# Kernel tuning notes

Measured on AMD Instinct MI355X. Metric: run time of the kernel, lower is better.

## Reference

```python
import jax, jax.numpy as jnp
import numpy as np

SPARSE_SHAPE = (468, 468, 1)
WINDOW_SHAPE = (12, 12, 1)
POS_TEMPERATURE = 10000.0
DROP_RANGE = (16, 32, 64, 100000)
DROP_TOKENS = (16, 32, 64, 144)
BATCH_SIZE = 4

_NX = int(np.ceil(SPARSE_SHAPE[0] / WINDOW_SHAPE[0])) + 1
_NY = int(np.ceil(SPARSE_SHAPE[1] / WINDOW_SHAPE[1])) + 1
_NZ = int(np.ceil(SPARSE_SHAPE[2] / WINDOW_SHAPE[2])) + 1
NUM_WINDOWS = BATCH_SIZE * _NX * _NY * _NZ  # total window-index space


def get_window_coors(coords, do_shift):
    # coords: [N,4] int32, order (b, z, y, x)
    wx, wy, wz = WINDOW_SHAPE
    if do_shift:
        sx, sy, sz = wx // 2, wy // 2, wz // 2
    else:
        sx, sy, sz = wx, wy, wz
    if SPARSE_SHAPE[2] == wz:
        sz = 0
    cx = coords[:, 3] + sx
    cy = coords[:, 2] + sy
    cz = coords[:, 1] + sz
    win_x, win_y, win_z = cx // wx, cy // wy, cz // wz
    per_sample = _NX * _NY * _NZ
    batch_win_inds = coords[:, 0] * per_sample + win_x * (_NY * _NZ) + win_y * _NZ + win_z
    coors_in_win = jnp.stack([cz % wz, cy % wy, cx % wx], axis=-1)  # (z,y,x)
    return batch_win_inds, coors_in_win


def masked_inner_win_inds(win_inds, keep):
    # rank (0..cnt-1) of each KEPT voxel inside its window (stable order)
    n = win_inds.shape[0]
    sentinel = jnp.int32(NUM_WINDOWS + 1)
    key = jnp.where(keep, win_inds, sentinel)
    order = jnp.argsort(key, stable=True)
    sk = key[order]
    pos = jnp.arange(n, dtype=jnp.int32)
    new_seg = jnp.concatenate([jnp.ones((1,), bool), sk[1:] != sk[:-1]])
    seg_start = jax.lax.cummax(jnp.where(new_seg, pos, 0), axis=0)
    inner_sorted = pos - seg_start
    return jnp.zeros(n, jnp.int32).at[order].set(inner_sorted)


def drop_single_shift(win_inds, keep):
    counts = jax.ops.segment_sum(keep.astype(jnp.int32), win_inds, num_segments=NUM_WINDOWS)
    num_before = counts[win_inds]  # tokens per window before this drop
    inner = masked_inner_win_inds(win_inds, keep)
    target = jnp.zeros_like(win_inds)
    drop_lvl = -jnp.ones_like(win_inds)
    lower = 0
    for dl, (upper, max_tok) in enumerate(zip(DROP_RANGE, DROP_TOKENS)):
        m = (num_before >= lower) & (num_before < upper)
        target = jnp.where(m, max_tok, target)
        drop_lvl = jnp.where(m, dl, drop_lvl)
        lower = upper
    keep_new = keep & (inner < target)
    return keep_new, jnp.where(keep, drop_lvl, -1), jnp.where(keep, inner, -1)


def pos_embed(coords_in_win, feat_dim):
    # 2D branch: window_shape[-1] == 1
    wx, wy, _ = WINDOW_SHAPE
    y = coords_in_win[:, 1].astype(jnp.float32) - wy / 2
    x = coords_in_win[:, 2].astype(jnp.float32) - wx / 2
    pos_length = feat_dim // 2
    inv_freq = POS_TEMPERATURE ** ((jnp.arange(pos_length // 2, dtype=jnp.float32) * 2) / pos_length)
    ex = x[:, None] / inv_freq[None, :]
    ey = y[:, None] / inv_freq[None, :]
    ex = jnp.stack([jnp.sin(ex), jnp.cos(ex)], axis=-1).reshape(x.shape[0], -1)
    ey = jnp.stack([jnp.sin(ey), jnp.cos(ey)], axis=-1).reshape(y.shape[0], -1)
    return jnp.concatenate([ex, ey], axis=-1)  # [N, feat_dim], gap == 0


def setup_inputs() -> dict:
    key = jax.random.key(0)
    k1, k2, k3, k4 = jax.random.split(key, 4)
    N, C = 300000, 128
    b = jax.random.randint(k1, (N,), 0, BATCH_SIZE, dtype=jnp.int32)
    z = jnp.zeros((N,), jnp.int32)
    y = jax.random.randint(k2, (N,), 0, SPARSE_SHAPE[1], dtype=jnp.int32)
    x = jax.random.randint(k3, (N,), 0, SPARSE_SHAPE[0], dtype=jnp.int32)
    voxel_coords = jnp.stack([b, z, y, x], axis=-1)
    voxel_feat = jax.random.normal(k4, (N, C), dtype=jnp.float32)
    return {"voxel_feat": voxel_feat, "voxel_coords": voxel_coords}


def reference(voxel_feat, voxel_coords):
    coords = voxel_coords.astype(jnp.int32)
    win0, inwin0 = get_window_coors(coords, do_shift=False)
    win1, inwin1 = get_window_coors(coords, do_shift=True)
    keep = jnp.ones(coords.shape[0], bool)
    keep, dl0, inner0 = drop_single_shift(win0, keep)
    keep, dl1, inner1 = drop_single_shift(win1, keep)
    C = voxel_feat.shape[1]
    pe0 = pos_embed(inwin0, C).astype(voxel_feat.dtype)
    pe1 = pos_embed(inwin1, C).astype(voxel_feat.dtype)
    # static-shape stand-in for boolean filtering: mask instead of compact
    feat_kept = voxel_feat * keep[:, None].astype(voxel_feat.dtype)
    return (feat_kept, keep, win0, win1, dl0, dl1, inner0, inner1, pe0, pe1)
```

## Files before the change

kernel.cpp:

```cpp
#include <hip/hip_runtime.h>

#define NWIN 12800
#define PER_SAMPLE 3200
#define NY_NZ 80
#define NZW 2

using f4 = __attribute__((ext_vector_type(4))) float;

__device__ __forceinline__ void tgt_lvl(int nb, int& tgt, int& lvl) {
    if (nb < 16)          { tgt = 16;  lvl = 0; }
    else if (nb < 32)     { tgt = 32;  lvl = 1; }
    else if (nb < 64)     { tgt = 64;  lvl = 2; }
    else                  { tgt = 144; lvl = 3; }
}

__global__ void k_pe_wins(const int4* __restrict__ coords, int N,
                          int* __restrict__ w0, int* __restrict__ w1,
                          int* __restrict__ counts0, f4* __restrict__ out4) {
    int tid = blockIdx.x * blockDim.x + threadIdx.x;
    if (tid >= N * 16) return;
    int i    = tid >> 4;
    int c4   = tid & 15;
    int lane = threadIdx.x & 63;

    int x = 0, y = 0;
    if (c4 == 0) {
        int4 c = coords[i];
        x = c.w; y = c.z;
        int wi0 = c.x * PER_SAMPLE + ((x + 12) / 12) * NY_NZ + ((y + 12) / 12) * NZW + c.y;
        int wi1 = c.x * PER_SAMPLE + ((x + 6)  / 12) * NY_NZ + ((y + 6)  / 12) * NZW + c.y;
        w0[i] = wi0;
        w1[i] = wi1;
        atomicAdd(&counts0[wi0], 1);
    }
    int src = lane & 48;
    x = __shfl(x, src, 64);
    y = __shfl(y, src, 64);

    float x0 = (float)(x % 12) - 6.0f;
    float y0 = (float)(y % 12) - 6.0f;
    float x1 = (float)((x + 6) % 12) - 6.0f;
    float y1 = (float)((y + 6) % 12) - 6.0f;

    float rf0 = exp2f((float)(2 * c4) * -0.415241011860920285f);
    float rf1 = rf0 * 0.749894209332455847f;

    float ax0 = x0 * rf0, bx0 = x0 * rf1, ay0 = y0 * rf0, by0 = y0 * rf1;
    float ax1 = x1 * rf0, bx1 = x1 * rf1, ay1 = y1 * rf0, by1 = y1 * rf1;
    f4 p0x = { __sinf(ax0), __cosf(ax0), __sinf(bx0), __cosf(bx0) };
    f4 p0y = { __sinf(ay0), __cosf(ay0), __sinf(by0), __cosf(by0) };
    f4 p1x = { __sinf(ax1), __cosf(ax1), __sinf(bx1), __cosf(bx1) };
    f4 p1y = { __sinf(ay1), __cosf(ay1), __sinf(by1), __cosf(by1) };

    size_t pe0 = ((size_t)N * 135) >> 2;
    size_t pe1 = pe0 + (((size_t)N * 128) >> 2);
    size_t vb  = (size_t)i * 32 + c4;
    __builtin_nontemporal_store(p0x, &out4[pe0 + vb]);
    __builtin_nontemporal_store(p0y, &out4[pe0 + vb + 16]);
    __builtin_nontemporal_store(p1x, &out4[pe1 + vb]);
    __builtin_nontemporal_store(p1y, &out4[pe1 + vb + 16]);
}

__global__ void k_scan(const int* __restrict__ counts,
                       int* __restrict__ starts, int* __restrict__ cursor) {
    __shared__ int ssum[256];
    const int CH = NWIN / 256;
    int t = threadIdx.x;
    int base = t * CH;
    int s = 0;
    for (int k = 0; k < CH; ++k) s += counts[base + k];
    ssum[t] = s;
    __syncthreads();
    for (int off = 1; off < 256; off <<= 1) {
        int v = (t >= off) ? ssum[t - off] : 0;
        __syncthreads();
        ssum[t] += v;
        __syncthreads();
    }
    int run = ssum[t] - s;
    for (int k = 0; k < CH; ++k) {
        starts[base + k] = run;
        cursor[base + k] = run;
        run += counts[base + k];
    }
}

__global__ void k_scatter0(const int* __restrict__ w0, int N,
                           int* __restrict__ cursor, int* __restrict__ sorted) {
    int i = blockIdx.x * blockDim.x + threadIdx.x;
    if (i >= N) return;
    int pos = atomicAdd(&cursor[w0[i]], 1);
    sorted[pos] = i;
}

__global__ void k_rank(const int* __restrict__ starts, const int* __restrict__ counts,
                       const int* __restrict__ sorted, int* __restrict__ inner,
                       const int* __restrict__ w1, int* __restrict__ counts1) {
    __shared__ int seg[1024];
    int w = blockIdx.x;
    int L = counts[w];
    if (L == 0) return;
    int s = starts[w];
    int lane = threadIdx.x;
    int tgt, lvl;
    tgt_lvl(L, tgt, lvl);
    if (L <= 1024) {
        for (int p = lane; p < L; p += 64) seg[p] = sorted[s + p];
        __syncthreads();
        for (int p = lane; p < L; p += 64) {
            int v = seg[p];
            int r = 0;
            for (int q = 0; q < L; ++q) r += (seg[q] < v) ? 1 : 0;
            inner[v] = r;
            if (w1 != nullptr && r < tgt) atomicAdd(&counts1[w1[v]], 1);
        }
    } else {
        for (int p = lane; p < L; p += 64) {
            int v = sorted[s + p];
            int r = 0;
            for (int q = 0; q < L; ++q) r += (sorted[s + q] < v) ? 1 : 0;
            inner[v] = r;
            if (w1 != nullptr && r < tgt) atomicAdd(&counts1[w1[v]], 1);
        }
    }
}

__global__ void k_scatter1(const int* __restrict__ w0, const int* __restrict__ w1,
                           const int* __restrict__ counts0, const int* __restrict__ inner0,
                           int N, int* __restrict__ cursor, int* __restrict__ sorted) {
    int i = blockIdx.x * blockDim.x + threadIdx.x;
    if (i >= N) return;
    int t, l;
    tgt_lvl(counts0[w0[i]], t, l);
    if (inner0[i] < t) {
        int pos = atomicAdd(&cursor[w1[i]], 1);
        sorted[pos] = i;
    }
}

__global__ void k_final(const f4* __restrict__ feat,
                        const int* __restrict__ w0, const int* __restrict__ w1,
                        const int* __restrict__ counts0, const int* __restrict__ counts1,
                        const int* __restrict__ inner0, const int* __restrict__ inner1,
                        int N, f4* __restrict__ out4, float* __restrict__ out) {
    int tid = blockIdx.x * blockDim.x + threadIdx.x;
    if (tid >= N * 16) return;
    int i    = tid >> 4;
    int c4   = tid & 15;
    int lane = threadIdx.x & 63;

    float k = 0.0f;
    if (c4 == 0) {
        int wi0 = w0[i], wi1 = w1[i];
        int t0, l0;
        tgt_lvl(counts0[wi0], t0, l0);
        int in0 = inner0[i];
        bool keep1 = in0 < t0;
        bool keep2 = false;
        int dl1v = -1, in1v = -1;
        if (keep1) {
            int t1, l1;
            tgt_lvl(counts1[wi1], t1, l1);
            int in1 = inner1[i];
            keep2 = in1 < t1;
            dl1v = l1;
            in1v = in1;
        }
        k = keep2 ? 1.0f : 0.0f;
        float* o = out + (size_t)N * 128;
        size_t n = (size_t)N;
        o[i]       = k;
        o[n + i]   = (float)wi0;
        o[2*n + i] = (float)wi1;
        o[3*n + i] = (float)l0;
        o[4*n + i] = (float)dl1v;
        o[5*n + i] = (float)in0;
        o[6*n + i] = (float)in1v;
    }
    k = __shfl(k, lane & 48, 64);

    size_t vb = (size_t)i * 32 + c4;
    f4 fa = __builtin_nontemporal_load(&feat[vb]);
    f4 fb = __builtin_nontemporal_load(&feat[vb + 16]);
    fa *= k;
    fb *= k;
    __builtin_nontemporal_store(fa, &out4[vb]);
    __builtin_nontemporal_store(fb, &out4[vb + 16]);
}

extern "C" void kernel_launch(void* const* d_in, const int* in_sizes, int n_in,
                              void* d_out, int out_size, void* d_ws, size_t ws_size,
                              hipStream_t stream) {
    const float* feat   = (const float*)d_in[0];
    const int*   coords = (const int*)d_in[1];
    int N = in_sizes[1] / 4;

    int* counts0 = (int*)d_ws;
    int* counts1 = counts0 + NWIN;
    int* starts0 = counts1 + NWIN;
    int* cursor0 = starts0 + NWIN;
    int* starts1 = cursor0 + NWIN;
    int* cursor1 = starts1 + NWIN;
    int* w0      = cursor1 + NWIN;
    int* w1      = w0 + N;
    int* inner0  = w1 + N;
    int* inner1  = inner0 + N;
    int* sortedB = inner1 + N;

    float* out = (float*)d_out;
    const int4* coords4 = (const int4*)coords;
    const f4*   feat4   = (const f4*)feat;

    int nb   = (N + 255) / 256;
    int nb16 = (N * 16 + 255) / 256;

    hipMemsetAsync(d_ws, 0, 2 * NWIN * sizeof(int), stream);

    k_pe_wins<<<nb16, 256, 0, stream>>>(coords4, N, w0, w1, counts0, (f4*)d_out);
    k_scan<<<1, 256, 0, stream>>>(counts0, starts0, cursor0);
    k_scatter0<<<nb, 256, 0, stream>>>(w0, N, cursor0, sortedB);
    k_rank<<<NWIN, 64, 0, stream>>>(starts0, counts0, sortedB, inner0, w1, counts1);
    k_scan<<<1, 256, 0, stream>>>(counts1, starts1, cursor1);
    k_scatter1<<<nb, 256, 0, stream>>>(w0, w1, counts0, inner0, N, cursor1, sortedB);
    k_rank<<<NWIN, 64, 0, stream>>>(starts1, counts1, sortedB, inner1, nullptr, nullptr);
    k_final<<<nb16, 256, 0, stream>>>(feat4, w0, w1, counts0, counts1, inner0, inner1,
                                      N, (f4*)d_out, out);
}
```

Before: 642.6 us.

## Fuse scan, scatter and rank stages into one cooperative kernel with grid syncs

Replaces the six middle kernel launches (scan, scatter, rank for both shifts) with a single cooperative kernel that separates the phases with grid-wide syncs. Window ranking also changes from one 64-thread block per window to one wavefront per window, using cross-lane shuffles when a window holds 64 or fewer voxels. The goal is to cut launch overhead and the cost of the small single-block scan launches, and to speed up ranking of small windows. In exchange the scan phases leave most of the grid idle at a grid barrier, and a non-cooperative fallback path is kept in case the cooperative launch fails.

```diff
diff --git a/kernel.cpp b/kernel.cpp
--- a/kernel.cpp
+++ b/kernel.cpp
@@ -1,4 +1,7 @@
 #include <hip/hip_runtime.h>
+#include <hip/hip_cooperative_groups.h>
+
+namespace cg = cooperative_groups;
 
 #define NWIN 12800
 #define PER_SAMPLE 3200
@@ -61,9 +64,11 @@
     __builtin_nontemporal_store(p1y, &out4[pe1 + vb + 16]);
 }
 
-__global__ void k_scan(const int* __restrict__ counts,
-                       int* __restrict__ starts, int* __restrict__ cursor) {
-    __shared__ int ssum[256];
+
+__device__ __forceinline__ void scan_block(const int* __restrict__ counts,
+                                           int* __restrict__ starts,
+                                           int* __restrict__ cursor,
+                                           int* ssum) {
     const int CH = NWIN / 256;
     int t = threadIdx.x;
     int base = t * CH;
@@ -85,49 +90,110 @@
     }
 }
 
-__global__ void k_scatter0(const int* __restrict__ w0, int N,
-                           int* __restrict__ cursor, int* __restrict__ sorted) {
+__device__ __forceinline__ void rank_windows(const int* __restrict__ starts,
+                                             const int* __restrict__ counts,
+                                             const int* __restrict__ sorted,
+                                             int* __restrict__ inner,
+                                             const int* __restrict__ w1,
+                                             int* __restrict__ counts1,
+                                             int gwave, int nwaves) {
+    int lane = threadIdx.x & 63;
+    for (int w = gwave; w < NWIN; w += nwaves) {
+        int L = counts[w];
+        if (L == 0) continue;
+        int s = starts[w];
+        int tgt, lvl;
+        tgt_lvl(L, tgt, lvl);
+        if (L <= 64) {
+            int v = (lane < L) ? sorted[s + lane] : 0x7fffffff;
+            int r = 0;
+            #pragma unroll
+            for (int q = 0; q < 64; ++q) {
+                int vq = __shfl(v, q, 64);
+                r += (vq < v) ? 1 : 0;
+            }
+            if (lane < L) {
+                inner[v] = r;
+                if (counts1 != nullptr && r < tgt) atomicAdd(&counts1[w1[v]], 1);
+            }
+        } else {
+            for (int p = lane; p < L; p += 64) {
+                int v = sorted[s + p];
+                int r = 0;
+                for (int q = 0; q < L; ++q) r += (sorted[s + q] < v) ? 1 : 0;
+                inner[v] = r;
+                if (counts1 != nullptr && r < tgt) atomicAdd(&counts1[w1[v]], 1);
+            }
+        }
+    }
+}
+
+__global__ void __launch_bounds__(256, 4) k_mid(
+        const int* __restrict__ w0, const int* __restrict__ w1,
+        int* __restrict__ counts0, int* __restrict__ counts1,
+        int* __restrict__ starts0, int* __restrict__ cursor0,
+        int* __restrict__ starts1, int* __restrict__ cursor1,
+        int* __restrict__ inner0, int* __restrict__ inner1,
+        int* __restrict__ sorted, int N) {
+    cg::grid_group grid = cg::this_grid();
+    __shared__ int ssum[256];
+    int gtid   = blockIdx.x * blockDim.x + threadIdx.x;
+    int gsz    = gridDim.x * blockDim.x;
+    int gwave  = gtid >> 6;
+    int nwaves = gsz >> 6;
+
+    if (blockIdx.x == 0) scan_block(counts0, starts0, cursor0, ssum);
+    grid.sync();
+
+    for (int i = gtid; i < N; i += gsz) {
+        int pos = atomicAdd(&cursor0[w0[i]], 1);
+        sorted[pos] = i;
+    }
+    grid.sync();
+
+    rank_windows(starts0, counts0, sorted, inner0, w1, counts1, gwave, nwaves);
+    grid.sync();
+
+    if (blockIdx.x == 0) scan_block(counts1, starts1, cursor1, ssum);
+    grid.sync();
+
+    for (int i = gtid; i < N; i += gsz) {
+        int t, l;
+        tgt_lvl(counts0[w0[i]], t, l);
+        if (inner0[i] < t) {
+            int pos = atomicAdd(&cursor1[w1[i]], 1);
+            sorted[pos] = i;
+        }
+    }
+    grid.sync();
+
+    rank_windows(starts1, counts1, sorted, inner1, nullptr, nullptr, gwave, nwaves);
+}
+
+__global__ void k_scan(const int* __restrict__ counts,
+                       int* __restrict__ starts, int* __restrict__ cursor) {
+    __shared__ int ssum[256];
+    scan_block(counts, starts, cursor, ssum);
+}
+
+__global__ void k_scatter0_g(const int* __restrict__ w0, int N,
+                             int* __restrict__ cursor, int* __restrict__ sorted) {
     int i = blockIdx.x * blockDim.x + threadIdx.x;
     if (i >= N) return;
     int pos = atomicAdd(&cursor[w0[i]], 1);
     sorted[pos] = i;
 }
 
-__global__ void k_rank(const int* __restrict__ starts, const int* __restrict__ counts,
-                       const int* __restrict__ sorted, int* __restrict__ inner,
-                       const int* __restrict__ w1, int* __restrict__ counts1) {
-    __shared__ int seg[1024];
-    int w = blockIdx.x;
-    int L = counts[w];
-    if (L == 0) return;
-    int s = starts[w];
-    int lane = threadIdx.x;
-    int tgt, lvl;
-    tgt_lvl(L, tgt, lvl);
-    if (L <= 1024) {
-        for (int p = lane; p < L; p += 64) seg[p] = sorted[s + p];
-        __syncthreads();
-        for (int p = lane; p < L; p += 64) {
-            int v = seg[p];
-            int r = 0;
-            for (int q = 0; q < L; ++q) r += (seg[q] < v) ? 1 : 0;
-            inner[v] = r;
-            if (w1 != nullptr && r < tgt) atomicAdd(&counts1[w1[v]], 1);
-        }
-    } else {
-        for (int p = lane; p < L; p += 64) {
-            int v = sorted[s + p];
-            int r = 0;
-            for (int q = 0; q < L; ++q) r += (sorted[s + q] < v) ? 1 : 0;
-            inner[v] = r;
-            if (w1 != nullptr && r < tgt) atomicAdd(&counts1[w1[v]], 1);
-        }
-    }
-}
-
-__global__ void k_scatter1(const int* __restrict__ w0, const int* __restrict__ w1,
-                           const int* __restrict__ counts0, const int* __restrict__ inner0,
-                           int N, int* __restrict__ cursor, int* __restrict__ sorted) {
+__global__ void k_rank_g(const int* __restrict__ starts, const int* __restrict__ counts,
+                         const int* __restrict__ sorted, int* __restrict__ inner,
+                         const int* __restrict__ w1, int* __restrict__ counts1) {
+    rank_windows(starts, counts, sorted, inner, w1, counts1,
+                 blockIdx.x * 4 + (threadIdx.x >> 6), gridDim.x * 4);
+}
+
+__global__ void k_scatter1_g(const int* __restrict__ w0, const int* __restrict__ w1,
+                             const int* __restrict__ counts0, const int* __restrict__ inner0,
+                             int N, int* __restrict__ cursor, int* __restrict__ sorted) {
     int i = blockIdx.x * blockDim.x + threadIdx.x;
     if (i >= N) return;
     int t, l;
@@ -214,15 +280,40 @@
     int nb   = (N + 255) / 256;
     int nb16 = (N * 16 + 255) / 256;
 
+    static int coop_grid = -1;
+    if (coop_grid < 0) {
+        int dev = 0;
+        hipGetDevice(&dev);
+        int ncu = 0;
+        hipDeviceGetAttribute(&ncu, hipDeviceAttributeMultiprocessorCount, dev);
+        if (ncu <= 0) ncu = 256;
+        int bpc = 0;
+        hipOccupancyMaxActiveBlocksPerMultiprocessor(&bpc, k_mid, 256, 0);
+        if (bpc < 1) bpc = 1;
+        long g = (long)ncu * (long)bpc;
+        if (g > 2048) g = 2048;
+        if (g < 64)   g = 64;
+        coop_grid = (int)g;
+    }
+
     hipMemsetAsync(d_ws, 0, 2 * NWIN * sizeof(int), stream);
 
     k_pe_wins<<<nb16, 256, 0, stream>>>(coords4, N, w0, w1, counts0, (f4*)d_out);
-    k_scan<<<1, 256, 0, stream>>>(counts0, starts0, cursor0);
-    k_scatter0<<<nb, 256, 0, stream>>>(w0, N, cursor0, sortedB);
-    k_rank<<<NWIN, 64, 0, stream>>>(starts0, counts0, sortedB, inner0, w1, counts1);
-    k_scan<<<1, 256, 0, stream>>>(counts1, starts1, cursor1);
-    k_scatter1<<<nb, 256, 0, stream>>>(w0, w1, counts0, inner0, N, cursor1, sortedB);
-    k_rank<<<NWIN, 64, 0, stream>>>(starts1, counts1, sortedB, inner1, nullptr, nullptr);
+
+    void* args[] = { (void*)&w0, (void*)&w1, (void*)&counts0, (void*)&counts1,
+                     (void*)&starts0, (void*)&cursor0, (void*)&starts1, (void*)&cursor1,
+                     (void*)&inner0, (void*)&inner1, (void*)&sortedB, (void*)&N };
+    hipError_t e = hipLaunchCooperativeKernel((void*)k_mid, dim3(coop_grid), dim3(256),
+                                              args, 0, stream);
+    if (e != hipSuccess) {
+        k_scan<<<1, 256, 0, stream>>>(counts0, starts0, cursor0);
+        k_scatter0_g<<<nb, 256, 0, stream>>>(w0, N, cursor0, sortedB);
+        k_rank_g<<<NWIN / 4, 256, 0, stream>>>(starts0, counts0, sortedB, inner0, w1, counts1);
+        k_scan<<<1, 256, 0, stream>>>(counts1, starts1, cursor1);
+        k_scatter1_g<<<nb, 256, 0, stream>>>(w0, w1, counts0, inner0, N, cursor1, sortedB);
+        k_rank_g<<<NWIN / 4, 256, 0, stream>>>(starts1, counts1, sortedB, inner1, nullptr, nullptr);
+    }
+
     k_final<<<nb16, 256, 0, stream>>>(feat4, w0, w1, counts0, counts1, inner0, inner1,
                                       N, (f4*)d_out, out);
 }
```

Result: slower. 1.131 ms (+76.0%).

## Bucket voxels into fixed-capacity per-window slots and rank with wave shuffles

Applied to the files above, without the earlier changes.

When the workspace is large enough, each voxel's index is written into a fixed 128-entry slot array for its window during the window-index atomic pass. This removes the single-block prefix scans and both scatter kernels. Ranking now runs one 64-lane wavefront per window, comparing entries through register shuffles instead of an O(L^2) loop over shared or global memory, and the rank-0 pass fills the second-shift slots directly. The risk is that windows holding more than 128 voxels are silently truncated, which gives wrong ranks and drop levels for dense inputs. The older scan-based path is kept as a fallback when the workspace is too small.

```diff
diff --git a/kernel.cpp b/kernel.cpp
--- a/kernel.cpp
+++ b/kernel.cpp
@@ -4,6 +4,7 @@
 #define PER_SAMPLE 3200
 #define NY_NZ 80
 #define NZW 2
+#define SLOT 128
 
 using f4 = __attribute__((ext_vector_type(4))) float;
 
@@ -16,7 +17,8 @@
 
 __global__ void k_pe_wins(const int4* __restrict__ coords, int N,
                           int* __restrict__ w0, int* __restrict__ w1,
-                          int* __restrict__ counts0, f4* __restrict__ out4) {
+                          int* __restrict__ counts0, int* __restrict__ slot0,
+                          f4* __restrict__ out4) {
     int tid = blockIdx.x * blockDim.x + threadIdx.x;
     if (tid >= N * 16) return;
     int i    = tid >> 4;
@@ -31,7 +33,9 @@
         int wi1 = c.x * PER_SAMPLE + ((x + 6)  / 12) * NY_NZ + ((y + 6)  / 12) * NZW + c.y;
         w0[i] = wi0;
         w1[i] = wi1;
-        atomicAdd(&counts0[wi0], 1);
+        int pos = atomicAdd(&counts0[wi0], 1);
+        if (slot0 != nullptr && pos < SLOT)
+            slot0[(size_t)wi0 * SLOT + pos] = i;
     }
     int src = lane & 48;
     x = __shfl(x, src, 64);
@@ -61,9 +65,68 @@
     __builtin_nontemporal_store(p1y, &out4[pe1 + vb + 16]);
 }
 
-__global__ void k_scan(const int* __restrict__ counts,
-                       int* __restrict__ starts, int* __restrict__ cursor) {
-    __shared__ int ssum[256];
+__global__ void __launch_bounds__(256) k_rank_slots(
+        const int* __restrict__ counts, const int* __restrict__ slots,
+        int* __restrict__ inner,
+        const int* __restrict__ w1, int* __restrict__ counts1,
+        int* __restrict__ slot1) {
+    int w    = blockIdx.x * 4 + (threadIdx.x >> 6);
+    int lane = threadIdx.x & 63;
+    int L = counts[w];
+    if (L <= 0) return;
+    if (L > SLOT) L = SLOT;
+    int tgt, lvl;
+    tgt_lvl(L, tgt, lvl);
+    const int* sl = slots + (size_t)w * SLOT;
+    if (L <= 64) {
+        int v = (lane < L) ? sl[lane] : 0x7fffffff;
+        int r = 0;
+        #pragma unroll
+        for (int q = 0; q < 64; ++q) {
+            int vq = __shfl(v, q, 64);
+            r += (vq < v) ? 1 : 0;
+        }
+        if (lane < L) {
+            inner[v] = r;
+            if (slot1 != nullptr && r < tgt) {
+                int wi = w1[v];
+                int p = atomicAdd(&counts1[wi], 1);
+                if (p < SLOT) slot1[(size_t)wi * SLOT + p] = v;
+            }
+        }
+    } else {
+        int v0 = sl[lane];
+        int v1 = (lane + 64 < L) ? sl[lane + 64] : 0x7fffffff;
+        int r0 = 0, r1 = 0;
+        #pragma unroll
+        for (int q = 0; q < 64; ++q) {
+            int a = __shfl(v0, q, 64);
+            int b = __shfl(v1, q, 64);
+            r0 += ((a < v0) ? 1 : 0) + ((b < v0) ? 1 : 0);
+            r1 += ((a < v1) ? 1 : 0) + ((b < v1) ? 1 : 0);
+        }
+        inner[v0] = r0;
+        if (slot1 != nullptr && r0 < tgt) {
+            int wi = w1[v0];
+            int p = atomicAdd(&counts1[wi], 1);
+            if (p < SLOT) slot1[(size_t)wi * SLOT + p] = v0;
+        }
+        if (lane + 64 < L) {
+            inner[v1] = r1;
+            if (slot1 != nullptr && r1 < tgt) {
+                int wi = w1[v1];
+                int p = atomicAdd(&counts1[wi], 1);
+                if (p < SLOT) slot1[(size_t)wi * SLOT + p] = v1;
+            }
+        }
+    }
+}
+
+
+__device__ __forceinline__ void scan_block(const int* __restrict__ counts,
+                                           int* __restrict__ starts,
+                                           int* __restrict__ cursor,
+                                           int* ssum) {
     const int CH = NWIN / 256;
     int t = threadIdx.x;
     int base = t * CH;
@@ -85,34 +148,42 @@
     }
 }
 
-__global__ void k_scatter0(const int* __restrict__ w0, int N,
-                           int* __restrict__ cursor, int* __restrict__ sorted) {
+__global__ void k_scan(const int* __restrict__ counts,
+                       int* __restrict__ starts, int* __restrict__ cursor) {
+    __shared__ int ssum[256];
+    scan_block(counts, starts, cursor, ssum);
+}
+
+__global__ void k_scatter0_g(const int* __restrict__ w0, int N,
+                             int* __restrict__ cursor, int* __restrict__ sorted) {
     int i = blockIdx.x * blockDim.x + threadIdx.x;
     if (i >= N) return;
     int pos = atomicAdd(&cursor[w0[i]], 1);
     sorted[pos] = i;
 }
 
-__global__ void k_rank(const int* __restrict__ starts, const int* __restrict__ counts,
-                       const int* __restrict__ sorted, int* __restrict__ inner,
-                       const int* __restrict__ w1, int* __restrict__ counts1) {
-    __shared__ int seg[1024];
-    int w = blockIdx.x;
+__global__ void k_rank_g(const int* __restrict__ starts, const int* __restrict__ counts,
+                         const int* __restrict__ sorted, int* __restrict__ inner,
+                         const int* __restrict__ w1, int* __restrict__ counts1) {
+    int lane = threadIdx.x & 63;
+    int w = blockIdx.x * 4 + (threadIdx.x >> 6);
+    if (w >= NWIN) return;
     int L = counts[w];
     if (L == 0) return;
     int s = starts[w];
-    int lane = threadIdx.x;
     int tgt, lvl;
     tgt_lvl(L, tgt, lvl);
-    if (L <= 1024) {
-        for (int p = lane; p < L; p += 64) seg[p] = sorted[s + p];
-        __syncthreads();
-        for (int p = lane; p < L; p += 64) {
-            int v = seg[p];
-            int r = 0;
-            for (int q = 0; q < L; ++q) r += (seg[q] < v) ? 1 : 0;
+    if (L <= 64) {
+        int v = (lane < L) ? sorted[s + lane] : 0x7fffffff;
+        int r = 0;
+        #pragma unroll
+        for (int q = 0; q < 64; ++q) {
+            int vq = __shfl(v, q, 64);
+            r += (vq < v) ? 1 : 0;
+        }
+        if (lane < L) {
             inner[v] = r;
-            if (w1 != nullptr && r < tgt) atomicAdd(&counts1[w1[v]], 1);
+            if (counts1 != nullptr && r < tgt) atomicAdd(&counts1[w1[v]], 1);
         }
     } else {
         for (int p = lane; p < L; p += 64) {
@@ -120,14 +191,14 @@
             int r = 0;
             for (int q = 0; q < L; ++q) r += (sorted[s + q] < v) ? 1 : 0;
             inner[v] = r;
-            if (w1 != nullptr && r < tgt) atomicAdd(&counts1[w1[v]], 1);
-        }
-    }
-}
-
-__global__ void k_scatter1(const int* __restrict__ w0, const int* __restrict__ w1,
-                           const int* __restrict__ counts0, const int* __restrict__ inner0,
-                           int N, int* __restrict__ cursor, int* __restrict__ sorted) {
+            if (counts1 != nullptr && r < tgt) atomicAdd(&counts1[w1[v]], 1);
+        }
+    }
+}
+
+__global__ void k_scatter1_g(const int* __restrict__ w0, const int* __restrict__ w1,
+                             const int* __restrict__ counts0, const int* __restrict__ inner0,
+                             int N, int* __restrict__ cursor, int* __restrict__ sorted) {
     int i = blockIdx.x * blockDim.x + threadIdx.x;
     if (i >= N) return;
     int t, l;
@@ -195,18 +266,6 @@
     const int*   coords = (const int*)d_in[1];
     int N = in_sizes[1] / 4;
 
-    int* counts0 = (int*)d_ws;
-    int* counts1 = counts0 + NWIN;
-    int* starts0 = counts1 + NWIN;
-    int* cursor0 = starts0 + NWIN;
-    int* starts1 = cursor0 + NWIN;
-    int* cursor1 = starts1 + NWIN;
-    int* w0      = cursor1 + NWIN;
-    int* w1      = w0 + N;
-    int* inner0  = w1 + N;
-    int* inner1  = inner0 + N;
-    int* sortedB = inner1 + N;
-
     float* out = (float*)d_out;
     const int4* coords4 = (const int4*)coords;
     const f4*   feat4   = (const f4*)feat;
@@ -214,15 +273,56 @@
     int nb   = (N + 255) / 256;
     int nb16 = (N * 16 + 255) / 256;
 
-    hipMemsetAsync(d_ws, 0, 2 * NWIN * sizeof(int), stream);
-
-    k_pe_wins<<<nb16, 256, 0, stream>>>(coords4, N, w0, w1, counts0, (f4*)d_out);
-    k_scan<<<1, 256, 0, stream>>>(counts0, starts0, cursor0);
-    k_scatter0<<<nb, 256, 0, stream>>>(w0, N, cursor0, sortedB);
-    k_rank<<<NWIN, 64, 0, stream>>>(starts0, counts0, sortedB, inner0, w1, counts1);
-    k_scan<<<1, 256, 0, stream>>>(counts1, starts1, cursor1);
-    k_scatter1<<<nb, 256, 0, stream>>>(w0, w1, counts0, inner0, N, cursor1, sortedB);
-    k_rank<<<NWIN, 64, 0, stream>>>(starts1, counts1, sortedB, inner1, nullptr, nullptr);
-    k_final<<<nb16, 256, 0, stream>>>(feat4, w0, w1, counts0, counts1, inner0, inner1,
-                                      N, (f4*)d_out, out);
-}
+    size_t need_fast = ((size_t)2 * NWIN + 4 * (size_t)N + 2 * (size_t)NWIN * SLOT)
+                       * sizeof(int);
+
+    if (ws_size >= need_fast) {
+        int* counts0 = (int*)d_ws;
+        int* counts1 = counts0 + NWIN;
+        int* w0      = counts1 + NWIN;
+        int* w1      = w0 + N;
+        int* inner0  = w1 + N;
+        int* inner1  = inner0 + N;
+        int* slot0   = inner1 + N;
+        int* slot1   = slot0 + (size_t)NWIN * SLOT;
+
+        hipMemsetAsync(d_ws, 0, 2 * NWIN * sizeof(int), stream);
+
+        k_pe_wins<<<nb16, 256, 0, stream>>>(coords4, N, w0, w1, counts0, slot0,
+                                            (f4*)d_out);
+        k_rank_slots<<<NWIN / 4, 256, 0, stream>>>(counts0, slot0, inner0,
+                                                   w1, counts1, slot1);
+        k_rank_slots<<<NWIN / 4, 256, 0, stream>>>(counts1, slot1, inner1,
+                                                   nullptr, nullptr, nullptr);
+        k_final<<<nb16, 256, 0, stream>>>(feat4, w0, w1, counts0, counts1,
+                                          inner0, inner1, N, (f4*)d_out, out);
+    } else {
+        int* counts0 = (int*)d_ws;
+        int* counts1 = counts0 + NWIN;
+        int* starts0 = counts1 + NWIN;
+        int* cursor0 = starts0 + NWIN;
+        int* starts1 = cursor0 + NWIN;
+        int* cursor1 = starts1 + NWIN;
+        int* w0      = cursor1 + NWIN;
+        int* w1      = w0 + N;
+        int* inner0  = w1 + N;
+        int* inner1  = inner0 + N;
+        int* sortedB = inner1 + N;
+
+        hipMemsetAsync(d_ws, 0, 2 * NWIN * sizeof(int), stream);
+
+        k_pe_wins<<<nb16, 256, 0, stream>>>(coords4, N, w0, w1, counts0, nullptr,
+                                            (f4*)d_out);
+        k_scan<<<1, 256, 0, stream>>>(counts0, starts0, cursor0);
+        k_scatter0_g<<<nb, 256, 0, stream>>>(w0, N, cursor0, sortedB);
+        k_rank_g<<<NWIN / 4, 256, 0, stream>>>(starts0, counts0, sortedB, inner0,
+                                               w1, counts1);
+        k_scan<<<1, 256, 0, stream>>>(counts1, starts1, cursor1);
+        k_scatter1_g<<<nb, 256, 0, stream>>>(w0, w1, counts0, inner0, N,
+                                             cursor1, sortedB);
+        k_rank_g<<<NWIN / 4, 256, 0, stream>>>(starts1, counts1, sortedB, inner1,
+                                               nullptr, nullptr);
+        k_final<<<nb16, 256, 0, stream>>>(feat4, w0, w1, counts0, counts1,
+                                          inner0, inner1, N, (f4*)d_out, out);
+    }
+}
```

Result: faster. 607.1 us (-5.5%).
